# Performance work log

Hardware: AMD Instinct MI355X
Metric: run time of the kernel (lower is better)

Reference implementation:

```python
import jax, jax.numpy as jnp
import numpy as np
import math

EPS_LN = 1e-5
SCALE = 16.0  # cosine_sim_scale


def layer_norm(x, g):
    mean = jnp.mean(x, axis=-1, keepdims=True)
    var = jnp.var(x, axis=-1, keepdims=True)  # biased, matches unbiased=False
    return (x - mean) * jax.lax.rsqrt(var + EPS_LN) * g


def l2norm(t):
    n = jnp.linalg.norm(t, axis=-1, keepdims=True)
    return t / jnp.maximum(n, 1e-12)


def setup_inputs() -> dict:
    key = jax.random.key(0)
    ks = jax.random.split(key, 4)
    b, n, dim, h, dh = 4, 2048, 1024, 8, 64
    inner = h * dh
    x = jax.random.normal(ks[0], (b, n, dim), dtype=jnp.float32)
    Wq = jax.random.normal(ks[1], (dim, inner), dtype=jnp.float32) * (dim ** -0.5)
    Wkv = jax.random.normal(ks[2], (dim, 2 * dh), dtype=jnp.float32) * (dim ** -0.5)
    Wout = jax.random.normal(ks[3], (inner, dim), dtype=jnp.float32) * (inner ** -0.5)
    norm_g = jnp.ones((dim,), dtype=jnp.float32)
    out_norm_g = jnp.ones((dim,), dtype=jnp.float32)
    return {"x": x, "norm_g": norm_g, "Wq": Wq, "Wkv": Wkv, "Wout": Wout,
            "out_norm_g": out_norm_g}


def reference(x, norm_g, Wq, Wkv, Wout, out_norm_g):
    b, n, dim = x.shape
    h = 8
    dh = Wkv.shape[-1] // 2
    xn = layer_norm(x, norm_g)
    q = xn @ Wq                      # [b, n, h*dh]
    kv = xn @ Wkv                    # [b, n, 2*dh]
    k, v = kv[..., :dh], kv[..., dh:]
    q = q.reshape(b, n, h, dh).transpose(0, 2, 1, 3)  # [b, h, n, dh]
    q = q * SCALE                    # cancelled by l2norm, kept for fidelity
    q = l2norm(q)
    k = l2norm(k)
    rs = math.sqrt(SCALE)
    q = q * rs
    k = k * rs
    sim = jnp.einsum('bhid,bjd->bhij', q, k)          # [b, h, n, n]
    attn = jax.nn.softmax(sim.astype(jnp.float32), axis=-1).astype(sim.dtype)
    out = jnp.einsum('bhij,bjd->bhid', attn, v)       # [b, h, n, dh]
    out = out.transpose(0, 2, 1, 3).reshape(b, n, h * dh)
    out = out @ Wout
    return layer_norm(out, out_norm_g)
```

## Files before the change

kernel.cpp:

```cpp
#include <hip/hip_runtime.h>
#include <hip/hip_bf16.h>

typedef __attribute__((ext_vector_type(8))) short short8;
typedef __attribute__((ext_vector_type(4))) float floatx4;
typedef __attribute__((ext_vector_type(16))) float floatx16;

__device__ __forceinline__ float bf2f(ushort u) {
    return __uint_as_float(((unsigned int)u) << 16);
}
__device__ __forceinline__ ushort f2bf(float f) {
    unsigned int u = __float_as_uint(f);
    unsigned int r = (u + 0x7FFFu + ((u >> 16) & 1u)) >> 16;
    return (ushort)r;
}
__device__ __forceinline__ unsigned int pk2(float a, float b) {
    union { __hip_bfloat162 h; unsigned int u; } cv;
    cv.h = __float22bfloat162_rn(make_float2(a, b));
    return cv.u;
}
__device__ __forceinline__ float scrub(float v, float lim) {
    return fminf(fmaxf(v, -lim), lim);
}
__device__ __forceinline__ void glds16(const ushort* g, ushort* l) {
    __builtin_amdgcn_global_load_lds((const __attribute__((address_space(1))) void*)g,
                                     (__attribute__((address_space(3))) void*)l, 16, 0, 0);
}

__device__ __forceinline__ bool detect_bf16(const ushort* __restrict__ probe) {
    const int lane = threadIdx.x & 63;
    ushort u = probe[(lane & 31) * 2];
    int e = (u >> 7) & 0xFF;
    bool pl = (e >= 117) && (e <= 131) && (lane < 32);
    return __popcll(__ballot(pl)) >= 16;
}

__device__ __forceinline__ void do_transpose(const void* __restrict__ in,
                                             ushort* __restrict__ out,
                                             int bx, int by, int in_rs, int out_rs,
                                             bool ib, ushort* tile ) {
    const int tx = threadIdx.x & 31, ty = threadIdx.x >> 5;
    #pragma unroll
    for (int rr = 0; rr < 32; rr += 8) {
        size_t idx = (size_t)(by * 32 + ty + rr) * in_rs + bx * 32 + tx;
        float v = ib ? bf2f(((const ushort*)in)[idx]) : ((const float*)in)[idx];
        tile[(ty + rr) * 33 + tx] = f2bf(scrub(v, 1e8f));
    }
    __syncthreads();
    #pragma unroll
    for (int rr = 0; rr < 32; rr += 8) {
        int r = bx * 32 + ty + rr;
        int c = by * 32 + tx;
        out[(size_t)r * out_rs + c] = tile[tx * 33 + (ty + rr)];
    }
}

__global__ __launch_bounds__(256) void prep_kernel(const void* __restrict__ xin,
                                                   const void* __restrict__ gin,
                                                   const void* __restrict__ Wq,
                                                   const void* __restrict__ Wkv,
                                                   ushort* __restrict__ xn,
                                                   ushort* __restrict__ wcatT,
                                                   const ushort* __restrict__ probe) {
    const bool ib = detect_bf16(probe);
    const int id = blockIdx.x;
    __shared__ ushort tile[32 * 33];
    __shared__ float red[8];

    if (id >= 8192) {
        if (id < 8704) {
            int t = id - 8192;
            do_transpose(Wq, wcatT, t & 15, t >> 4, 512, 1024, ib, tile);
        } else {
            int t = id - 8704;
            do_transpose(Wkv, wcatT + (size_t)512 * 1024, t & 3, t >> 2, 128, 1024, ib, tile);
        }
        return;
    }

    const int row = id;
    const int tid = threadIdx.x;
    float v0, v1, v2, v3, g0, g1, g2, g3;
    if (ib) {
        uint2 u = *(const uint2*)((const ushort*)xin + (size_t)row * 1024 + tid * 4);
        v0 = bf2f((ushort)(u.x & 0xFFFF)); v1 = bf2f((ushort)(u.x >> 16));
        v2 = bf2f((ushort)(u.y & 0xFFFF)); v3 = bf2f((ushort)(u.y >> 16));
        uint2 gu = *(const uint2*)((const ushort*)gin + tid * 4);
        g0 = bf2f((ushort)(gu.x & 0xFFFF)); g1 = bf2f((ushort)(gu.x >> 16));
        g2 = bf2f((ushort)(gu.y & 0xFFFF)); g3 = bf2f((ushort)(gu.y >> 16));
    } else {
        float4 xv = *(const float4*)((const float*)xin + (size_t)row * 1024 + tid * 4);
        v0 = xv.x; v1 = xv.y; v2 = xv.z; v3 = xv.w;
        float4 gv = *(const float4*)((const float*)gin + tid * 4);
        g0 = gv.x; g1 = gv.y; g2 = gv.z; g3 = gv.w;
    }
    v0 = scrub(v0, 1e8f); v1 = scrub(v1, 1e8f); v2 = scrub(v2, 1e8f); v3 = scrub(v3, 1e8f);
    g0 = scrub(g0, 1e8f); g1 = scrub(g1, 1e8f); g2 = scrub(g2, 1e8f); g3 = scrub(g3, 1e8f);

    float s  = v0 + v1 + v2 + v3;
    float sq = v0 * v0 + v1 * v1 + v2 * v2 + v3 * v3;
    #pragma unroll
    for (int off = 1; off < 64; off <<= 1) {
        s  += __shfl_xor(s, off);
        sq += __shfl_xor(sq, off);
    }
    const int w = tid >> 6, lane = tid & 63;
    if (lane == 0) { red[w] = s; red[w + 4] = sq; }
    __syncthreads();
    float S  = red[0] + red[1] + red[2] + red[3];
    float SQ = red[4] + red[5] + red[6] + red[7];

    float mean = S * (1.0f / 1024.0f);
    float var  = SQ * (1.0f / 1024.0f) - mean * mean;
    float rstd = rsqrtf(fmaxf(var, 0.0f) + 1e-5f);

    uint2 ov;
    ov.x = pk2((v0 - mean) * rstd * g0, (v1 - mean) * rstd * g1);
    ov.y = pk2((v2 - mean) * rstd * g2, (v3 - mean) * rstd * g3);
    *(uint2*)(xn + (size_t)row * 1024 + tid * 4) = ov;
}

__global__ __launch_bounds__(256) void wout_tr_kernel(const void* __restrict__ Wout,
                                                      ushort* __restrict__ woT,
                                                      const ushort* __restrict__ probe) {
    const bool ib = detect_bf16(probe);
    __shared__ ushort tile[32 * 33];
    do_transpose(Wout, woT, blockIdx.x, blockIdx.y, 1024, 512, ib, tile);
}

__global__ __launch_bounds__(256) void ln2_kernel(const ushort* __restrict__ y,
                                                  const void* __restrict__ gin,
                                                  void* __restrict__ out,
                                                  const ushort* __restrict__ probe) {
    const bool ob = detect_bf16(probe);
    const int row = blockIdx.x;
    const int tid = threadIdx.x;

    uint2 u = *(const uint2*)(y + (size_t)row * 1024 + tid * 4);
    float v0 = scrub(bf2f((ushort)(u.x & 0xFFFF)), 1e8f);
    float v1 = scrub(bf2f((ushort)(u.x >> 16)),    1e8f);
    float v2 = scrub(bf2f((ushort)(u.y & 0xFFFF)), 1e8f);
    float v3 = scrub(bf2f((ushort)(u.y >> 16)),    1e8f);

    float g0, g1, g2, g3;
    if (ob) {
        uint2 gu = *(const uint2*)((const ushort*)gin + tid * 4);
        g0 = bf2f((ushort)(gu.x & 0xFFFF)); g1 = bf2f((ushort)(gu.x >> 16));
        g2 = bf2f((ushort)(gu.y & 0xFFFF)); g3 = bf2f((ushort)(gu.y >> 16));
    } else {
        float4 gv = *(const float4*)((const float*)gin + tid * 4);
        g0 = gv.x; g1 = gv.y; g2 = gv.z; g3 = gv.w;
    }
    g0 = scrub(g0, 1e8f); g1 = scrub(g1, 1e8f); g2 = scrub(g2, 1e8f); g3 = scrub(g3, 1e8f);

    float s  = v0 + v1 + v2 + v3;
    float sq = v0 * v0 + v1 * v1 + v2 * v2 + v3 * v3;
    #pragma unroll
    for (int off = 1; off < 64; off <<= 1) {
        s  += __shfl_xor(s, off);
        sq += __shfl_xor(sq, off);
    }
    __shared__ float red[8];
    const int w = tid >> 6, lane = tid & 63;
    if (lane == 0) { red[w] = s; red[w + 4] = sq; }
    __syncthreads();
    float S  = red[0] + red[1] + red[2] + red[3];
    float SQ = red[4] + red[5] + red[6] + red[7];

    float mean = S * (1.0f / 1024.0f);
    float var  = SQ * (1.0f / 1024.0f) - mean * mean;
    float rstd = rsqrtf(fmaxf(var, 0.0f) + 1e-5f);

    float o0 = (v0 - mean) * rstd * g0;
    float o1 = (v1 - mean) * rstd * g1;
    float o2 = (v2 - mean) * rstd * g2;
    float o3 = (v3 - mean) * rstd * g3;
    if (ob) {
        uint2 ov;
        ov.x = pk2(o0, o1);
        ov.y = pk2(o2, o3);
        *(uint2*)((ushort*)out + (size_t)row * 1024 + tid * 4) = ov;
    } else {
        *(float4*)((float*)out + (size_t)row * 1024 + tid * 4) = make_float4(o0, o1, o2, o3);
    }
}

__global__ __launch_bounds__(256) void gemm_qkv(const ushort* __restrict__ A,
                                                const ushort* __restrict__ Bt,
                                                ushort* __restrict__ qb,
                                                ushort* __restrict__ kb,
                                                ushort* __restrict__ vt) {
    __shared__ ushort a_t[64 * 32];
    __shared__ ushort b_t[64 * 32];

    const int bx = blockIdx.x;
    const int n0 = bx * 64, m0 = blockIdx.y * 64;
    const int tid = threadIdx.x;
    const int w = tid >> 6, lane = tid & 63;
    const int fm = lane & 15, quad = lane >> 4;
    const int K = 1024;

    const ushort* ag = A + (size_t)(m0 + (tid >> 2)) * K + (tid & 3) * 8;
    const ushort* bg = Bt + (size_t)(n0 + (tid >> 2)) * K + (tid & 3) * 8;
    ushort* la = a_t + w * 512;
    ushort* lb = b_t + w * 512;

    floatx4 acc[4];
    floatx4 zero4 = {0.0f, 0.0f, 0.0f, 0.0f};
    #pragma unroll
    for (int nt = 0; nt < 4; nt++) acc[nt] = zero4;

    union U8 { uint4 u4; short8 s8; };

    for (int k0 = 0; k0 < K; k0 += 32) {
        __syncthreads();
        glds16(ag + k0, la);
        glds16(bg + k0, lb);
        __syncthreads();

        U8 af;
        af.u4 = *(const uint4*)&a_t[(w * 16 + fm) * 32 + quad * 8];
        #pragma unroll
        for (int nt = 0; nt < 4; nt++) {
            U8 bf;
            bf.u4 = *(const uint4*)&b_t[(nt * 16 + fm) * 32 + quad * 8];
            acc[nt] = __builtin_amdgcn_mfma_f32_16x16x32_bf16(af.s8, bf.s8, acc[nt], 0, 0, 0);
        }
    }

    if (bx < 9) {
        const float qsc = (bx < 8) ? 5.7707801636f : 4.0f;
        float sc[4];
        #pragma unroll
        for (int r = 0; r < 4; r++) {
            float ss = acc[0][r] * acc[0][r] + acc[1][r] * acc[1][r]
                     + acc[2][r] * acc[2][r] + acc[3][r] * acc[3][r];
            ss += __shfl_xor(ss, 1);
            ss += __shfl_xor(ss, 2);
            ss += __shfl_xor(ss, 4);
            ss += __shfl_xor(ss, 8);
            sc[r] = qsc / fmaxf(sqrtf(ss), 1e-12f);
        }
        ushort* op;
        int rs;
        if (bx < 8) { op = qb + n0; rs = 512; }
        else        { op = kb;      rs = 64;  }
        #pragma unroll
        for (int nt = 0; nt < 4; nt++)
            #pragma unroll
            for (int r = 0; r < 4; r++)
                op[(size_t)(m0 + w * 16 + quad * 4 + r) * rs + nt * 16 + fm] =
                    f2bf(acc[nt][r] * sc[r]);
    } else {
        const int b = m0 >> 11;
        const int jb = (m0 & 2047) + w * 16 + quad * 4;
        ushort* vb = vt + (size_t)b * 64 * 2048 + jb;
        #pragma unroll
        for (int nt = 0; nt < 4; nt++) {
            uint2 pv;
            pv.x = pk2(acc[nt][0], acc[nt][1]);
            pv.y = pk2(acc[nt][2], acc[nt][3]);
            *(uint2*)(vb + (size_t)(nt * 16 + fm) * 2048) = pv;
        }
    }
}

__global__ __launch_bounds__(256) void gemm_bt128(const ushort* __restrict__ A,
                                                  const ushort* __restrict__ Bt,
                                                  ushort* __restrict__ C,
                                                  int M, int N, int K) {
    __shared__ ushort a_t[128][32];
    __shared__ ushort b_t[128][32];

    const int n0 = blockIdx.x * 128, m0 = blockIdx.y * 128;
    const int tid = threadIdx.x;
    const int w = tid >> 6, lane = tid & 63;
    const int fm = lane & 15, quad = lane >> 4;

    const int c0 = tid, c1 = tid + 256;
    const ushort* ag0 = A + (size_t)(m0 + (c0 >> 2)) * K + (c0 & 3) * 8;
    const ushort* ag1 = A + (size_t)(m0 + (c1 >> 2)) * K + (c1 & 3) * 8;
    const ushort* bg0 = Bt + (size_t)(n0 + (c0 >> 2)) * K + (c0 & 3) * 8;
    const ushort* bg1 = Bt + (size_t)(n0 + (c1 >> 2)) * K + (c1 & 3) * 8;
    ushort* la0 = &a_t[0][0] + w * 512;
    ushort* la1 = &a_t[0][0] + 2048 + w * 512;
    ushort* lb0 = &b_t[0][0] + w * 512;
    ushort* lb1 = &b_t[0][0] + 2048 + w * 512;

    floatx4 acc[2][8];
    floatx4 zero4 = {0.0f, 0.0f, 0.0f, 0.0f};
    #pragma unroll
    for (int mt = 0; mt < 2; mt++)
        #pragma unroll
        for (int nt = 0; nt < 8; nt++) acc[mt][nt] = zero4;

    union U8 { uint4 u4; short8 s8; };

    for (int k0 = 0; k0 < K; k0 += 32) {
        __syncthreads();
        glds16(ag0 + k0, la0);
        glds16(ag1 + k0, la1);
        glds16(bg0 + k0, lb0);
        glds16(bg1 + k0, lb1);
        __syncthreads();

        U8 af[2];
        #pragma unroll
        for (int mt = 0; mt < 2; mt++)
            af[mt].u4 = *(const uint4*)&a_t[w * 32 + mt * 16 + fm][quad * 8];
        #pragma unroll
        for (int nt = 0; nt < 8; nt++) {
            U8 bf;
            bf.u4 = *(const uint4*)&b_t[nt * 16 + fm][quad * 8];
            acc[0][nt] = __builtin_amdgcn_mfma_f32_16x16x32_bf16(af[0].s8, bf.s8, acc[0][nt], 0, 0, 0);
            acc[1][nt] = __builtin_amdgcn_mfma_f32_16x16x32_bf16(af[1].s8, bf.s8, acc[1][nt], 0, 0, 0);
        }
    }

    #pragma unroll
    for (int mt = 0; mt < 2; mt++)
        #pragma unroll
        for (int nt = 0; nt < 8; nt++)
            #pragma unroll
            for (int r = 0; r < 4; r++)
                C[(size_t)(m0 + w * 32 + mt * 16 + quad * 4 + r) * N + n0 + nt * 16 + fm] =
                    f2bf(acc[mt][nt][r]);
}

__global__ __launch_bounds__(256, 2) void attn_kernel(const ushort* __restrict__ q,
                                                      const ushort* __restrict__ kb,
                                                      const ushort* __restrict__ vt,
                                                      ushort* __restrict__ out) {
    __shared__ ushort k_t[2][64 * 64];
    __shared__ ushort v_t[2][64 * 64];

    const int i0 = blockIdx.x * 128;
    const int h0 = blockIdx.y, b = blockIdx.z;
    const int tid = threadIdx.x, w = tid >> 6, lane = tid & 63;
    const int cq = lane & 31;
    const int hi = lane >> 5;
    const int sw = cq & 7;

    union U8 { uint4 u4; short8 s8; };

    const ushort* qbase = q + (size_t)(b * 2048 + i0 + w * 32 + cq) * 512 + h0 * 64 + hi * 8;
    U8 qf[4];
    #pragma unroll
    for (int dm = 0; dm < 4; dm++) qf[dm].u4 = *(const uint4*)(qbase + dm * 16);

    floatx16 acc0, acc1;
    #pragma unroll
    for (int i = 0; i < 16; i++) { acc0[i] = 0.0f; acc1[i] = 0.0f; }
    float lsum = 0.0f;

    const ushort* kbb = kb + (size_t)b * 2048 * 64;
    const ushort* vtb = vt + (size_t)b * 64 * 2048;

    const int srow0 = w * 16 + (lane >> 3);
    const int srow1 = srow0 + 8;
    const int soct = (lane & 7) ^ (srow0 & 7);
    const int prow0 = (srow0 & ~12) | ((srow0 & 4) << 1) | ((srow0 & 8) >> 1);
    const int prow1 = (srow1 & ~12) | ((srow1 & 4) << 1) | ((srow1 & 8) >> 1);
    const ushort* kgl0 = kbb + (size_t)prow0 * 64 + soct * 8;
    const ushort* kgl1 = kbb + (size_t)prow1 * 64 + soct * 8;
    const ushort* vgl0 = vtb + (size_t)srow0 * 2048 + soct * 8;
    const ushort* vgl1 = vtb + (size_t)srow1 * 2048 + soct * 8;
    ushort* kld = &k_t[0][0] + w * 1024;
    ushort* vld = &v_t[0][0] + w * 1024;

    int koff[4];
    #pragma unroll
    for (int i = 0; i < 4; i++) koff[i] = ((2 * i + hi) ^ sw) * 8;
    const int rb0 = cq * 64, rb1 = rb0 + 2048;

    auto stage = [&](int s, int bufo) {
        const size_t kj = (size_t)s * 4096;
        const int vj = s * 64;
        glds16(kgl0 + kj, kld + bufo);
        glds16(kgl1 + kj, kld + bufo + 512);
        glds16(vgl0 + vj, vld + bufo);
        glds16(vgl1 + vj, vld + bufo + 512);
    };

    auto compute = [&](const ushort* ktile, const ushort* vtile) {
        {
            U8 pb0, pb1;
            floatx16 st;
            #pragma unroll
            for (int i = 0; i < 16; i++) st[i] = -23.0831206f;
            #pragma unroll
            for (int dm = 0; dm < 4; dm++) {
                U8 kf;
                kf.u4 = *(const uint4*)&ktile[rb0 + koff[dm]];
                st = __builtin_amdgcn_mfma_f32_32x32x16_bf16(kf.s8, qf[dm].s8, st, 0, 0, 0);
            }
            float p_[16];
            #pragma unroll
            for (int r = 0; r < 16; r++) p_[r] = __builtin_amdgcn_exp2f(st[r]);
            lsum += (((p_[0] + p_[1]) + (p_[2] + p_[3])) + ((p_[4] + p_[5]) + (p_[6] + p_[7])))
                  + (((p_[8] + p_[9]) + (p_[10] + p_[11])) + ((p_[12] + p_[13]) + (p_[14] + p_[15])));
            pb0.u4.x = pk2(p_[0], p_[1]);   pb0.u4.y = pk2(p_[2], p_[3]);
            pb0.u4.z = pk2(p_[4], p_[5]);   pb0.u4.w = pk2(p_[6], p_[7]);
            pb1.u4.x = pk2(p_[8], p_[9]);   pb1.u4.y = pk2(p_[10], p_[11]);
            pb1.u4.z = pk2(p_[12], p_[13]); pb1.u4.w = pk2(p_[14], p_[15]);
            U8 vf;
            vf.u4 = *(const uint4*)&vtile[rb0 + koff[0]];
            acc0 = __builtin_amdgcn_mfma_f32_32x32x16_bf16(vf.s8, pb0.s8, acc0, 0, 0, 0);
            vf.u4 = *(const uint4*)&vtile[rb0 + koff[1]];
            acc0 = __builtin_amdgcn_mfma_f32_32x32x16_bf16(vf.s8, pb1.s8, acc0, 0, 0, 0);
            vf.u4 = *(const uint4*)&vtile[rb1 + koff[0]];
            acc1 = __builtin_amdgcn_mfma_f32_32x32x16_bf16(vf.s8, pb0.s8, acc1, 0, 0, 0);
            vf.u4 = *(const uint4*)&vtile[rb1 + koff[1]];
            acc1 = __builtin_amdgcn_mfma_f32_32x32x16_bf16(vf.s8, pb1.s8, acc1, 0, 0, 0);
        }
        {
            U8 pb2, pb3;
            floatx16 st;
            #pragma unroll
            for (int i = 0; i < 16; i++) st[i] = -23.0831206f;
            #pragma unroll
            for (int dm = 0; dm < 4; dm++) {
                U8 kf;
                kf.u4 = *(const uint4*)&ktile[rb1 + koff[dm]];
                st = __builtin_amdgcn_mfma_f32_32x32x16_bf16(kf.s8, qf[dm].s8, st, 0, 0, 0);
            }
            float p_[16];
            #pragma unroll
            for (int r = 0; r < 16; r++) p_[r] = __builtin_amdgcn_exp2f(st[r]);
            lsum += (((p_[0] + p_[1]) + (p_[2] + p_[3])) + ((p_[4] + p_[5]) + (p_[6] + p_[7])))
                  + (((p_[8] + p_[9]) + (p_[10] + p_[11])) + ((p_[12] + p_[13]) + (p_[14] + p_[15])));
            pb2.u4.x = pk2(p_[0], p_[1]);   pb2.u4.y = pk2(p_[2], p_[3]);
            pb2.u4.z = pk2(p_[4], p_[5]);   pb2.u4.w = pk2(p_[6], p_[7]);
            pb3.u4.x = pk2(p_[8], p_[9]);   pb3.u4.y = pk2(p_[10], p_[11]);
            pb3.u4.z = pk2(p_[12], p_[13]); pb3.u4.w = pk2(p_[14], p_[15]);
            U8 vf;
            vf.u4 = *(const uint4*)&vtile[rb0 + koff[2]];
            acc0 = __builtin_amdgcn_mfma_f32_32x32x16_bf16(vf.s8, pb2.s8, acc0, 0, 0, 0);
            vf.u4 = *(const uint4*)&vtile[rb0 + koff[3]];
            acc0 = __builtin_amdgcn_mfma_f32_32x32x16_bf16(vf.s8, pb3.s8, acc0, 0, 0, 0);
            vf.u4 = *(const uint4*)&vtile[rb1 + koff[2]];
            acc1 = __builtin_amdgcn_mfma_f32_32x32x16_bf16(vf.s8, pb2.s8, acc1, 0, 0, 0);
            vf.u4 = *(const uint4*)&vtile[rb1 + koff[3]];
            acc1 = __builtin_amdgcn_mfma_f32_32x32x16_bf16(vf.s8, pb3.s8, acc1, 0, 0, 0);
        }
    };

    stage(0, 0);
    __syncthreads();

    for (int s = 0; s < 32; s++) {
        const int cur = (s & 1) << 12;
        if (s < 31) stage(s + 1, cur ^ 4096);
        compute(&k_t[0][0] + cur, &v_t[0][0] + cur);
        __syncthreads();
    }

    lsum += __shfl_xor(lsum, 32);
    float li = 1.0f / fmaxf(lsum, 1e-30f);

    ushort* ob = out + (size_t)(b * 2048 + i0 + w * 32 + cq) * 512 + h0 * 64 + hi * 4;
    #pragma unroll
    for (int t = 0; t < 4; t++) {
        uint2 ov;
        ov.x = pk2(acc0[4 * t] * li, acc0[4 * t + 1] * li);
        ov.y = pk2(acc0[4 * t + 2] * li, acc0[4 * t + 3] * li);
        *(uint2*)(ob + t * 8) = ov;
        ov.x = pk2(acc1[4 * t] * li, acc1[4 * t + 1] * li);
        ov.y = pk2(acc1[4 * t + 2] * li, acc1[4 * t + 3] * li);
        *(uint2*)(ob + 32 + t * 8) = ov;
    }
}

extern "C" void kernel_launch(void* const* d_in, const int* in_sizes, int n_in,
                              void* d_out, int out_size, void* d_ws, size_t ws_size,
                              hipStream_t stream) {
    const void* x          = d_in[0];
    const void* norm_g     = d_in[1];
    const void* Wq         = d_in[2];
    const void* Wkv        = d_in[3];
    const void* Wout       = d_in[4];
    const void* out_norm_g = d_in[5];
    const ushort* probe = (const ushort*)d_in[0];
    ushort* ws = (ushort*)d_ws;

    const size_t M1 = 1024 * 1024 / 2;
    ushort* xn    = (ushort*)d_out;
    ushort* ao    = (ushort*)d_out;
    ushort* woT   = (ushort*)((char*)d_out + (8u << 20));
    ushort* qb    = ws;
    ushort* kb    = ws + 8 * M1;
    ushort* vt    = ws + 9 * M1;
    ushort* wcatT = ws + 11 * M1;
    ushort* y     = ws;

    prep_kernel<<<8832, 256, 0, stream>>>(x, norm_g, Wq, Wkv, xn, wcatT, probe);

    gemm_qkv<<<dim3(10, 128), 256, 0, stream>>>(xn, wcatT, qb, kb, vt);

    wout_tr_kernel<<<dim3(32, 16), 256, 0, stream>>>(Wout, woT, probe);

    attn_kernel<<<dim3(16, 8, 4), 256, 0, stream>>>(qb, kb, vt, ao);

    gemm_bt128<<<dim3(8, 64), 256, 0, stream>>>(ao, woT, y, 8192, 1024, 512);

    ln2_kernel<<<8192, 256, 0, stream>>>(y, out_norm_g, d_out, probe);
}
```

Before: 214.1 us.

## Split attention key range across wave pairs and halve query tile per block

The attention kernel now gives each block 64 queries instead of 128 and splits the key sequence between two wave pairs. Each pair processes half of the keys with 32-key steps and its own LDS layout. The two partial accumulators and row sums are combined through shared memory at the end. The grid doubles to 1024 blocks and launch bounds allow four blocks per CU, to raise occupancy and parallelism on the many-CU device. The cost is an extra reduction and sync, and twice as many per-step barriers relative to the work done per step.

```diff
diff --git a/kernel.cpp b/kernel.cpp
--- a/kernel.cpp
+++ b/kernel.cpp
@@ -326,23 +326,25 @@
                     f2bf(acc[mt][nt][r]);
 }
 
-__global__ __launch_bounds__(256, 2) void attn_kernel(const ushort* __restrict__ q,
+__global__ __launch_bounds__(256, 4) void attn_kernel(const ushort* __restrict__ q,
                                                       const ushort* __restrict__ kb,
                                                       const ushort* __restrict__ vt,
                                                       ushort* __restrict__ out) {
-    __shared__ ushort k_t[2][64 * 64];
-    __shared__ ushort v_t[2][64 * 64];
-
-    const int i0 = blockIdx.x * 128;
+    __shared__ ushort smem[16384];
+    ushort* k_t = smem;
+    ushort* v_t = smem + 8192;
+
+    const int i0 = blockIdx.x * 64;
     const int h0 = blockIdx.y, b = blockIdx.z;
     const int tid = threadIdx.x, w = tid >> 6, lane = tid & 63;
+    const int qg = w & 1;
+    const int ks = w >> 1;
     const int cq = lane & 31;
     const int hi = lane >> 5;
-    const int sw = cq & 7;
 
     union U8 { uint4 u4; short8 s8; };
 
-    const ushort* qbase = q + (size_t)(b * 2048 + i0 + w * 32 + cq) * 512 + h0 * 64 + hi * 8;
+    const ushort* qbase = q + (size_t)(b * 2048 + i0 + qg * 32 + cq) * 512 + h0 * 64 + hi * 8;
     U8 qf[4];
     #pragma unroll
     for (int dm = 0; dm < 4; dm++) qf[dm].u4 = *(const uint4*)(qbase + dm * 16);
@@ -355,109 +357,79 @@
     const ushort* kbb = kb + (size_t)b * 2048 * 64;
     const ushort* vtb = vt + (size_t)b * 64 * 2048;
 
-    const int srow0 = w * 16 + (lane >> 3);
-    const int srow1 = srow0 + 8;
-    const int soct = (lane & 7) ^ (srow0 & 7);
-    const int prow0 = (srow0 & ~12) | ((srow0 & 4) << 1) | ((srow0 & 8) >> 1);
-    const int prow1 = (srow1 & ~12) | ((srow1 & 4) << 1) | ((srow1 & 8) >> 1);
-    const ushort* kgl0 = kbb + (size_t)prow0 * 64 + soct * 8;
-    const ushort* kgl1 = kbb + (size_t)prow1 * 64 + soct * 8;
-    const ushort* vgl0 = vtb + (size_t)srow0 * 2048 + soct * 8;
-    const ushort* vgl1 = vtb + (size_t)srow1 * 2048 + soct * 8;
-    ushort* kld = &k_t[0][0] + w * 1024;
-    ushort* vld = &v_t[0][0] + w * 1024;
-
-    int koff[4];
-    #pragma unroll
-    for (int i = 0; i < 4; i++) koff[i] = ((2 * i + hi) ^ sw) * 8;
-    const int rb0 = cq * 64, rb1 = rb0 + 2048;
-
-    auto stage = [&](int s, int bufo) {
-        const size_t kj = (size_t)s * 4096;
-        const int vj = s * 64;
-        glds16(kgl0 + kj, kld + bufo);
-        glds16(kgl1 + kj, kld + bufo + 512);
-        glds16(vgl0 + vj, vld + bufo);
-        glds16(vgl1 + vj, vld + bufo + 512);
+    const int p5 = (cq & ~12) | ((cq & 4) << 1) | ((cq & 8) >> 1);
+    const ushort* kSrc = kbb + (size_t)(ks * 1024 + p5) * 64 + hi * 8;
+    const ushort* vSrc = vtb + (size_t)lane * 2048 + ks * 1024;
+
+    ushort* kT = k_t + ks * 4096;
+    ushort* vT = v_t + ks * 4096;
+
+    auto stage = [&](int s, int buf) {
+        const int bo = buf * 2048;
+        #pragma unroll
+        for (int c = 2 * qg; c < 2 * qg + 2; c++) {
+            glds16(kSrc + s * 2048 + c * 16, kT + bo + c * 512);
+            glds16(vSrc + s * 32 + c * 8,  vT + bo + c * 512);
+        }
     };
 
-    auto compute = [&](const ushort* ktile, const ushort* vtile) {
-        {
-            U8 pb0, pb1;
-            floatx16 st;
-            #pragma unroll
-            for (int i = 0; i < 16; i++) st[i] = -23.0831206f;
-            #pragma unroll
-            for (int dm = 0; dm < 4; dm++) {
-                U8 kf;
-                kf.u4 = *(const uint4*)&ktile[rb0 + koff[dm]];
-                st = __builtin_amdgcn_mfma_f32_32x32x16_bf16(kf.s8, qf[dm].s8, st, 0, 0, 0);
-            }
-            float p_[16];
-            #pragma unroll
-            for (int r = 0; r < 16; r++) p_[r] = __builtin_amdgcn_exp2f(st[r]);
-            lsum += (((p_[0] + p_[1]) + (p_[2] + p_[3])) + ((p_[4] + p_[5]) + (p_[6] + p_[7])))
-                  + (((p_[8] + p_[9]) + (p_[10] + p_[11])) + ((p_[12] + p_[13]) + (p_[14] + p_[15])));
-            pb0.u4.x = pk2(p_[0], p_[1]);   pb0.u4.y = pk2(p_[2], p_[3]);
-            pb0.u4.z = pk2(p_[4], p_[5]);   pb0.u4.w = pk2(p_[6], p_[7]);
-            pb1.u4.x = pk2(p_[8], p_[9]);   pb1.u4.y = pk2(p_[10], p_[11]);
-            pb1.u4.z = pk2(p_[12], p_[13]); pb1.u4.w = pk2(p_[14], p_[15]);
-            U8 vf;
-            vf.u4 = *(const uint4*)&vtile[rb0 + koff[0]];
-            acc0 = __builtin_amdgcn_mfma_f32_32x32x16_bf16(vf.s8, pb0.s8, acc0, 0, 0, 0);
-            vf.u4 = *(const uint4*)&vtile[rb0 + koff[1]];
-            acc0 = __builtin_amdgcn_mfma_f32_32x32x16_bf16(vf.s8, pb1.s8, acc0, 0, 0, 0);
-            vf.u4 = *(const uint4*)&vtile[rb1 + koff[0]];
-            acc1 = __builtin_amdgcn_mfma_f32_32x32x16_bf16(vf.s8, pb0.s8, acc1, 0, 0, 0);
-            vf.u4 = *(const uint4*)&vtile[rb1 + koff[1]];
-            acc1 = __builtin_amdgcn_mfma_f32_32x32x16_bf16(vf.s8, pb1.s8, acc1, 0, 0, 0);
-        }
-        {
-            U8 pb2, pb3;
-            floatx16 st;
-            #pragma unroll
-            for (int i = 0; i < 16; i++) st[i] = -23.0831206f;
-            #pragma unroll
-            for (int dm = 0; dm < 4; dm++) {
-                U8 kf;
-                kf.u4 = *(const uint4*)&ktile[rb1 + koff[dm]];
-                st = __builtin_amdgcn_mfma_f32_32x32x16_bf16(kf.s8, qf[dm].s8, st, 0, 0, 0);
-            }
-            float p_[16];
-            #pragma unroll
-            for (int r = 0; r < 16; r++) p_[r] = __builtin_amdgcn_exp2f(st[r]);
-            lsum += (((p_[0] + p_[1]) + (p_[2] + p_[3])) + ((p_[4] + p_[5]) + (p_[6] + p_[7])))
-                  + (((p_[8] + p_[9]) + (p_[10] + p_[11])) + ((p_[12] + p_[13]) + (p_[14] + p_[15])));
-            pb2.u4.x = pk2(p_[0], p_[1]);   pb2.u4.y = pk2(p_[2], p_[3]);
-            pb2.u4.z = pk2(p_[4], p_[5]);   pb2.u4.w = pk2(p_[6], p_[7]);
-            pb3.u4.x = pk2(p_[8], p_[9]);   pb3.u4.y = pk2(p_[10], p_[11]);
-            pb3.u4.z = pk2(p_[12], p_[13]); pb3.u4.w = pk2(p_[14], p_[15]);
-            U8 vf;
-            vf.u4 = *(const uint4*)&vtile[rb0 + koff[2]];
-            acc0 = __builtin_amdgcn_mfma_f32_32x32x16_bf16(vf.s8, pb2.s8, acc0, 0, 0, 0);
-            vf.u4 = *(const uint4*)&vtile[rb0 + koff[3]];
-            acc0 = __builtin_amdgcn_mfma_f32_32x32x16_bf16(vf.s8, pb3.s8, acc0, 0, 0, 0);
-            vf.u4 = *(const uint4*)&vtile[rb1 + koff[2]];
-            acc1 = __builtin_amdgcn_mfma_f32_32x32x16_bf16(vf.s8, pb2.s8, acc1, 0, 0, 0);
-            vf.u4 = *(const uint4*)&vtile[rb1 + koff[3]];
-            acc1 = __builtin_amdgcn_mfma_f32_32x32x16_bf16(vf.s8, pb3.s8, acc1, 0, 0, 0);
-        }
+    auto compute = [&](int buf) {
+        const int bo = buf * 2048;
+        floatx16 st;
+        #pragma unroll
+        for (int i = 0; i < 16; i++) st[i] = -23.0831206f;
+        #pragma unroll
+        for (int dm = 0; dm < 4; dm++) {
+            U8 kf;
+            kf.u4 = *(const uint4*)&kT[bo + (2 * dm + hi) * 256 + cq * 8];
+            st = __builtin_amdgcn_mfma_f32_32x32x16_bf16(kf.s8, qf[dm].s8, st, 0, 0, 0);
+        }
+        float p_[16];
+        #pragma unroll
+        for (int r = 0; r < 16; r++) p_[r] = __builtin_amdgcn_exp2f(st[r]);
+        lsum += (((p_[0] + p_[1]) + (p_[2] + p_[3])) + ((p_[4] + p_[5]) + (p_[6] + p_[7])))
+              + (((p_[8] + p_[9]) + (p_[10] + p_[11])) + ((p_[12] + p_[13]) + (p_[14] + p_[15])));
+        U8 pb0, pb1;
+        pb0.u4.x = pk2(p_[0], p_[1]);   pb0.u4.y = pk2(p_[2], p_[3]);
+        pb0.u4.z = pk2(p_[4], p_[5]);   pb0.u4.w = pk2(p_[6], p_[7]);
+        pb1.u4.x = pk2(p_[8], p_[9]);   pb1.u4.y = pk2(p_[10], p_[11]);
+        pb1.u4.z = pk2(p_[12], p_[13]); pb1.u4.w = pk2(p_[14], p_[15]);
+        U8 vf;
+        vf.u4 = *(const uint4*)&vT[bo + (0 + hi) * 512 + cq * 8];
+        acc0 = __builtin_amdgcn_mfma_f32_32x32x16_bf16(vf.s8, pb0.s8, acc0, 0, 0, 0);
+        vf.u4 = *(const uint4*)&vT[bo + (2 + hi) * 512 + cq * 8];
+        acc0 = __builtin_amdgcn_mfma_f32_32x32x16_bf16(vf.s8, pb1.s8, acc0, 0, 0, 0);
+        vf.u4 = *(const uint4*)&vT[bo + (0 + hi) * 512 + (32 + cq) * 8];
+        acc1 = __builtin_amdgcn_mfma_f32_32x32x16_bf16(vf.s8, pb0.s8, acc1, 0, 0, 0);
+        vf.u4 = *(const uint4*)&vT[bo + (2 + hi) * 512 + (32 + cq) * 8];
+        acc1 = __builtin_amdgcn_mfma_f32_32x32x16_bf16(vf.s8, pb1.s8, acc1, 0, 0, 0);
     };
 
     stage(0, 0);
     __syncthreads();
 
     for (int s = 0; s < 32; s++) {
-        const int cur = (s & 1) << 12;
-        if (s < 31) stage(s + 1, cur ^ 4096);
-        compute(&k_t[0][0] + cur, &v_t[0][0] + cur);
+        const int cur = s & 1;
+        if (s < 31) stage(s + 1, cur ^ 1);
+        compute(cur);
         __syncthreads();
     }
 
+    float* row = (float*)smem + (qg * 64 + lane) * 36;
+    if (ks == 1) {
+        #pragma unroll
+        for (int i = 0; i < 16; i++) { row[i] = acc0[i]; row[16 + i] = acc1[i]; }
+        row[32] = lsum;
+    }
+    __syncthreads();
+    if (ks == 1) return;
+    #pragma unroll
+    for (int i = 0; i < 16; i++) { acc0[i] += row[i]; acc1[i] += row[16 + i]; }
+    lsum += row[32];
     lsum += __shfl_xor(lsum, 32);
     float li = 1.0f / fmaxf(lsum, 1e-30f);
 
-    ushort* ob = out + (size_t)(b * 2048 + i0 + w * 32 + cq) * 512 + h0 * 64 + hi * 4;
+    ushort* ob = out + (size_t)(b * 2048 + i0 + qg * 32 + cq) * 512 + h0 * 64 + hi * 4;
     #pragma unroll
     for (int t = 0; t < 4; t++) {
         uint2 ov;
@@ -498,7 +470,7 @@
 
     wout_tr_kernel<<<dim3(32, 16), 256, 0, stream>>>(Wout, woT, probe);
 
-    attn_kernel<<<dim3(16, 8, 4), 256, 0, stream>>>(qb, kb, vt, ao);
+    attn_kernel<<<dim3(32, 8, 4), 256, 0, stream>>>(qb, kb, vt, ao);
 
     gemm_bt128<<<dim3(8, 64), 256, 0, stream>>>(ao, woT, y, 8192, 1024, 512);
 
```

Measured after the change: 227.0 us. 6.0% more time.
